# Kernel optimization log

Hardware: AMD Instinct MI355X
Metric: run time of the kernel (lower is better)

Reference implementation:

```python
import jax, jax.numpy as jnp
import numpy as np

HIDDEN = 1024
HEADS = 16
HEAD_DIM = HIDDEN // HEADS
MAX_SEQ = 2048
BATCH = 2
SEQ = 2048


def setup_inputs() -> dict:
    key = jax.random.key(0)
    ks = jax.random.split(key, 6)
    x = jax.random.normal(ks[0], (BATCH, SEQ, HIDDEN), dtype=jnp.float32)
    # torch Linear params expressed as [in, out] weight + bias
    W1 = jax.random.normal(ks[1], (HIDDEN, 4 * HIDDEN), dtype=jnp.float32) * (HIDDEN ** -0.5)
    b1 = jnp.zeros((4 * HIDDEN,), dtype=jnp.float32)
    W2 = jax.random.normal(ks[2], (HIDDEN, HIDDEN), dtype=jnp.float32) * (HIDDEN ** -0.5)
    b2 = jnp.zeros((HIDDEN,), dtype=jnp.float32)
    rel_table = jax.random.normal(ks[3], (2 * MAX_SEQ - 1, HEADS), dtype=jnp.float32) * 0.02
    # causal mask [B, S, S]; True = keep
    attn_mask = jnp.broadcast_to(jnp.tril(jnp.ones((SEQ, SEQ), dtype=bool)), (BATCH, SEQ, SEQ))
    return {"x": x, "W1": W1, "b1": b1, "W2": W2, "b2": b2,
            "rel_table": rel_table, "attn_mask": attn_mask}


def reference(x, W1, b1, W2, b2, rel_table, attn_mask):
    B, S, H = x.shape
    # fused projection + SiLU, then chunk into U, Q, K, V
    activated = jax.nn.silu(jnp.einsum('bsh,hf->bsf', x, W1) + b1)
    U, Qp, Kp, Vp = jnp.split(activated, 4, axis=-1)
    # [B, nH, S, hd]
    def heads(t):
        return t.reshape(B, S, HEADS, HEAD_DIM).transpose(0, 2, 1, 3)
    Q, K, V = heads(Qp), heads(Kp), heads(Vp)
    scale = HEAD_DIM ** -0.5
    scores = jnp.einsum('bnqd,bnkd->bnqk', Q, K) * scale
    # relative position bias gather: idx[i,j] = i - j + MAX_SEQ - 1
    pos = jnp.arange(S)
    rel_idx = pos[:, None] - pos[None, :] + (MAX_SEQ - 1)  # [S, S]
    rel_bias = rel_table[rel_idx].transpose(2, 0, 1)[None]  # [1, nH, S, S]
    scores = scores + rel_bias
    attn = jax.nn.silu(scores)
    attn = jnp.where(attn_mask[:, None, :, :], attn, 0.0)
    out = jnp.einsum('bnqk,bnkd->bnqd', attn, V)
    out = out.transpose(0, 2, 1, 3).reshape(B, S, H)
    gated = out * U
    return jnp.einsum('bsh,hf->bsf', gated, W2) + b2
```

## Files before the change

kernel.cpp:

```cpp
#include <hip/hip_runtime.h>
#include <hip/hip_bf16.h>
#include <math.h>

#define HIDDEN   1024
#define HEADS    16
#define HEAD_DIM 64
#define SEQ      2048
#define BATCH    2
#define FDIM     4096
#define MTOT     4096
#define MAXSEQ   2048

typedef __bf16 bf16x8 __attribute__((ext_vector_type(8)));
typedef float  f32x4  __attribute__((ext_vector_type(4)));
typedef unsigned short u16;

__device__ __forceinline__ float silu_fast(float v) {
    return v * __builtin_amdgcn_rcpf(1.f + __expf(-v));
}

__device__ __forceinline__ u16 f2bf(float f) {
    union { float f; unsigned u; } v; v.f = f;
    unsigned r = v.u + 0x7FFFu + ((v.u >> 16) & 1u);
    return (u16)(r >> 16);
}
__device__ __forceinline__ float bf2f(u16 b) {
    union { unsigned u; float f; } v; v.u = ((unsigned)b) << 16;
    return v.f;
}
__device__ __forceinline__ unsigned pk2(float a, float b) {
    union { __hip_bfloat162 h; unsigned u; } z;
    z.h = __float22bfloat162_rn(make_float2(a, b));
    return z.u;
}

__device__ __forceinline__ void gload16(const void* g, void* l) {
    __builtin_amdgcn_global_load_lds(
        (const __attribute__((address_space(1))) void*)g,
        (__attribute__((address_space(3))) void*)l, 16, 0, 0);
}

__global__ __launch_bounds__(256) void convert_x_kernel(
    const float* __restrict__ src, u16* __restrict__ dst)
{
    int idx = (blockIdx.x * 256 + threadIdx.x) * 8;
    float4 a = *(const float4*)&src[idx];
    float4 b = *(const float4*)&src[idx + 4];
    u16 h8[8] = {f2bf(a.x), f2bf(a.y), f2bf(a.z), f2bf(a.w),
                 f2bf(b.x), f2bf(b.y), f2bf(b.z), f2bf(b.w)};
    *(float4*)&dst[idx] = *(float4*)h8;
}

__global__ __launch_bounds__(256) void transpose_convert_kernel(
    const float* __restrict__ W, u16* __restrict__ Wt, int rows, int cols)
{
    __shared__ u16 T[64][72];
    const int tid = threadIdx.x;
    const int r0 = blockIdx.y * 64, c0 = blockIdx.x * 64;
#pragma unroll
    for (int l = 0; l < 4; ++l) {
        int idx = tid + l * 256;
        int row = idx >> 4;
        int c4  = (idx & 15) * 4;
        float4 v = *(const float4*)&W[(size_t)(r0 + row) * cols + c0 + c4];
        T[c4 + 0][row] = f2bf(v.x);
        T[c4 + 1][row] = f2bf(v.y);
        T[c4 + 2][row] = f2bf(v.z);
        T[c4 + 3][row] = f2bf(v.w);
    }
    __syncthreads();
#pragma unroll
    for (int l = 0; l < 2; ++l) {
        int idx = tid + l * 256;
        int row = idx >> 3;
        int cb  = (idx & 7) * 8;
        *(float4*)&Wt[(size_t)(c0 + row) * rows + r0 + cb] = *(float4*)&T[row][cb];
    }
}

#define GEMM_CORE(A_PTR, BT_PTR, KDIM, BM_, BN_, WMW, WNW)                     \
    enum { MTI = (BM_) / (WMW) / 16, NTI = (BN_) / (WNW) / 16,                 \
           ACH = (BM_) / 8, BCH = (BN_) / 8 };                                 \
    __shared__ __align__(16) u16 As[(BM_) * 64];                               \
    __shared__ __align__(16) u16 Bs[(BN_) * 64];                               \
    const int tid  = threadIdx.x;                                              \
    const int lane = tid & 63;                                                 \
    const int w    = tid >> 6;                                                 \
    const int wm   = w % (WMW), wn = w / (WMW);                                \
    const int l16  = lane & 15, quad = lane >> 4;                              \
    const int m0   = blockIdx.y * (BM_);                                       \
    const int n0   = blockIdx.x * (BN_);                                       \
    const int srow = lane >> 3;                                                \
    const int scol = (lane & 7) * 8;                                           \
    f32x4 acc[MTI][NTI];                                                       \
    _Pragma("unroll")                                                          \
    for (int mt = 0; mt < MTI; ++mt)                                           \
        _Pragma("unroll")                                                      \
        for (int nt = 0; nt < NTI; ++nt)                                       \
            acc[mt][nt] = (f32x4){0.f, 0.f, 0.f, 0.f};                         \
    for (int k0 = 0; k0 < (KDIM); k0 += 64) {                                  \
        __syncthreads();                                                       \
        _Pragma("unroll")                                                      \
        for (int ci = w; ci < ACH; ci += 4) {                                  \
            unsigned off = __builtin_amdgcn_readfirstlane(ci * 1024);          \
            gload16(&(A_PTR)[(size_t)(m0 + ci * 8 + srow) * (KDIM) + k0 + scol],\
                    (char*)As + off);                                          \
        }                                                                      \
        _Pragma("unroll")                                                      \
        for (int ci = w; ci < BCH; ci += 4) {                                  \
            unsigned off = __builtin_amdgcn_readfirstlane(ci * 1024);          \
            gload16(&(BT_PTR)[(size_t)(n0 + ci * 8 + srow) * (KDIM) + k0 + scol],\
                    (char*)Bs + off);                                          \
        }                                                                      \
        __syncthreads();                                                       \
        _Pragma("unroll")                                                      \
        for (int kc = 0; kc < 2; ++kc) {                                       \
            bf16x8 af[MTI], bfr[NTI];                                          \
            _Pragma("unroll")                                                  \
            for (int t = 0; t < MTI; ++t)                                      \
                af[t]  = *(const bf16x8*)&As[(wm * (BM_ / WMW) + t * 16 + l16) \
                                             * 64 + kc * 32 + quad * 8];       \
            _Pragma("unroll")                                                  \
            for (int t = 0; t < NTI; ++t)                                      \
                bfr[t] = *(const bf16x8*)&Bs[(wn * (BN_ / WNW) + t * 16 + l16) \
                                             * 64 + kc * 32 + quad * 8];       \
            _Pragma("unroll")                                                  \
            for (int mt = 0; mt < MTI; ++mt)                                   \
                _Pragma("unroll")                                              \
                for (int nt = 0; nt < NTI; ++nt)                               \
                    acc[mt][nt] = __builtin_amdgcn_mfma_f32_16x16x32_bf16(     \
                        bfr[nt], af[mt], acc[mt][nt], 0, 0, 0);                \
        }                                                                      \
    }

__global__ __launch_bounds__(256) void gemm1_mfma_kernel(
    const u16* __restrict__ A, const u16* __restrict__ Bt,
    const float* __restrict__ b1,
    u16* __restrict__ Ub, u16* __restrict__ Qh,
    u16* __restrict__ Kh, u16* __restrict__ Vh)
{
    GEMM_CORE(A, Bt, HIDDEN, 128, 128, 2, 2)

    const int chunk = n0 >> 10;
    u16* dstbase = (chunk == 0) ? Ub : (chunk == 1) ? Qh : (chunk == 2) ? Kh : Vh;
    const float postscale = (chunk == 1) ? 0.125f : 1.0f;

    float4 bias4[NTI]; int nloc[NTI];
#pragma unroll
    for (int nt = 0; nt < NTI; ++nt) {
        int nb = n0 + wn * 64 + nt * 16 + quad * 4;
        bias4[nt] = *(const float4*)&b1[nb];
        nloc[nt] = nb & 1023;
    }
#pragma unroll
    for (int mt = 0; mt < MTI; ++mt) {
        int m  = m0 + wm * 64 + mt * 16 + l16;
        int bb = m >> 11, s = m & 2047;
#pragma unroll
        for (int nt = 0; nt < NTI; ++nt) {
            float v0 = silu_fast(acc[mt][nt][0] + bias4[nt].x) * postscale;
            float v1 = silu_fast(acc[mt][nt][1] + bias4[nt].y) * postscale;
            float v2 = silu_fast(acc[mt][nt][2] + bias4[nt].z) * postscale;
            float v3 = silu_fast(acc[mt][nt][3] + bias4[nt].w) * postscale;
            uint2 pk = make_uint2(pk2(v0, v1), pk2(v2, v3));
            size_t o;
            if (chunk == 0) {
                o = (size_t)m * 1024 + nloc[nt];
            } else {
                int h = nloc[nt] >> 6, d = nloc[nt] & 63;
                o = (size_t)(((bb * HEADS + h) * SEQ) + s) * HEAD_DIM + d;
            }
            *(uint2*)&dstbase[o] = pk;
        }
    }
}

__global__ __launch_bounds__(256) void gemm2_mfma_kernel(
    const u16* __restrict__ A, const u16* __restrict__ Bt,
    const float* __restrict__ b2, float* __restrict__ Out)
{
    GEMM_CORE(A, Bt, HIDDEN, 64, 128, 1, 4)

    float4 bias4[NTI]; int nb[NTI];
#pragma unroll
    for (int nt = 0; nt < NTI; ++nt) {
        nb[nt] = n0 + wn * 32 + nt * 16 + quad * 4;
        bias4[nt] = *(const float4*)&b2[nb[nt]];
    }
#pragma unroll
    for (int mt = 0; mt < MTI; ++mt) {
        int m = m0 + mt * 16 + l16;
#pragma unroll
        for (int nt = 0; nt < NTI; ++nt) {
            float4 vv;
            vv.x = acc[mt][nt][0] + bias4[nt].x;
            vv.y = acc[mt][nt][1] + bias4[nt].y;
            vv.z = acc[mt][nt][2] + bias4[nt].z;
            vv.w = acc[mt][nt][3] + bias4[nt].w;
            *(float4*)&Out[(size_t)m * 1024 + nb[nt]] = vv;
        }
    }
}

#define PS 72

__global__ __launch_bounds__(256, 4) void attn_mfma_kernel(
    const u16* __restrict__ Qh, const u16* __restrict__ Kh,
    const u16* __restrict__ Vh, const float* __restrict__ rel,
    const u16* __restrict__ Ub, u16* __restrict__ G)
{
    __shared__ u16 Ks[64][PS];
    __shared__ u16 Vt[64][PS];
    __shared__ u16 Ps[64][PS];
    __shared__ float rel_sh[128];

    const int tid  = threadIdx.x;
    const int lane = tid & 63;
    const int w    = tid >> 6;
    const int quad = lane >> 4;
    const int l16  = lane & 15;

    const int bid   = blockIdx.x;
    const int x5    = bid & 31;
    const int h     = (bid >> 5) & 15;
    const int bb    = bid >> 9;
    const int phase = (bid >> 8) & 1;
    const int qt    = phase ? (31 - x5) : x5;
    const int q0    = qt * 64;

    const u16* Kg = Kh + (size_t)((bb * HEADS + h) * SEQ) * HEAD_DIM;
    const u16* Vg = Vh + (size_t)((bb * HEADS + h) * SEQ) * HEAD_DIM;
    const u16* Qg = Qh + (size_t)((bb * HEADS + h) * SEQ + q0) * HEAD_DIM;

    const int qrow = w * 16 + l16;
    bf16x8 qa0 = *(const bf16x8*)&Qg[qrow * HEAD_DIM + quad * 8];
    bf16x8 qa1 = *(const bf16x8*)&Qg[qrow * HEAD_DIM + 32 + quad * 8];

    const int k_r = tid >> 3,      k_c = (tid & 7) * 8;
    const int v_k = (tid & 31) * 2, v_d = (tid >> 5) * 8;

    float4 kreg0 = *(const float4*)&Kg[(size_t)k_r * HEAD_DIM + k_c];
    float4 kreg1 = *(const float4*)&Kg[(size_t)(k_r + 32) * HEAD_DIM + k_c];
    float4 vreg0 = *(const float4*)&Vg[(size_t)v_k * HEAD_DIM + v_d];
    float4 vreg1 = *(const float4*)&Vg[(size_t)(v_k + 1) * HEAD_DIM + v_d];
    float  relreg = 0.f;
    if (tid < 127) relreg = rel[(size_t)(q0 + 1984 + tid) * HEADS + h];

    f32x4 o[4];
#pragma unroll
    for (int dt = 0; dt < 4; ++dt) o[dt] = (f32x4){0.f, 0.f, 0.f, 0.f};

    for (int kt = 0; kt <= qt; ++kt) {
        *(float4*)&Ks[k_r][k_c]      = kreg0;
        *(float4*)&Ks[k_r + 32][k_c] = kreg1;
        {
            union { float4 f; u16 u[8]; } a0, a1;
            a0.f = vreg0; a1.f = vreg1;
#pragma unroll
            for (int i = 0; i < 8; ++i)
                *(unsigned*)&Vt[v_d + i][v_k] =
                    (unsigned)a0.u[i] | ((unsigned)a1.u[i] << 16);
        }
        if (tid < 127) rel_sh[tid] = relreg;
        __syncthreads();

        if (kt < qt) {
            const int kn = (kt + 1) * 64;
            kreg0 = *(const float4*)&Kg[(size_t)(kn + k_r) * HEAD_DIM + k_c];
            kreg1 = *(const float4*)&Kg[(size_t)(kn + k_r + 32) * HEAD_DIM + k_c];
            vreg0 = *(const float4*)&Vg[(size_t)(kn + v_k) * HEAD_DIM + v_d];
            vreg1 = *(const float4*)&Vg[(size_t)(kn + v_k + 1) * HEAD_DIM + v_d];
            if (tid < 127)
                relreg = rel[(size_t)(q0 - kn + 1984 + tid) * HEADS + h];
        }

        const int qrel = q0 - kt * 64 + qrow;

#pragma unroll
        for (int ct = 0; ct < 4; ++ct) {
            bf16x8 ka0 = *(const bf16x8*)&Ks[ct * 16 + l16][quad * 8];
            bf16x8 ka1 = *(const bf16x8*)&Ks[ct * 16 + l16][32 + quad * 8];
            f32x4 sc = {0.f, 0.f, 0.f, 0.f};
            sc = __builtin_amdgcn_mfma_f32_16x16x32_bf16(ka0, qa0, sc, 0, 0, 0);
            sc = __builtin_amdgcn_mfma_f32_16x16x32_bf16(ka1, qa1, sc, 0, 0, 0);
            float p[4];
#pragma unroll
            for (int r = 0; r < 4; ++r) {
                int kloc = ct * 16 + quad * 4 + r;
                float s  = sc[r] + rel_sh[qrow - kloc + 63];
                p[r] = (qrel - kloc >= 0) ? silu_fast(s) : 0.f;
            }
            uint2 pk = make_uint2(pk2(p[0], p[1]), pk2(p[2], p[3]));
            *(uint2*)&Ps[qrow][ct * 16 + quad * 4] = pk;
        }

        bf16x8 pa0 = *(const bf16x8*)&Ps[qrow][quad * 8];
        bf16x8 pa1 = *(const bf16x8*)&Ps[qrow][32 + quad * 8];
#pragma unroll
        for (int dt = 0; dt < 4; ++dt) {
            bf16x8 vb0 = *(const bf16x8*)&Vt[dt * 16 + l16][quad * 8];
            bf16x8 vb1 = *(const bf16x8*)&Vt[dt * 16 + l16][32 + quad * 8];
            o[dt] = __builtin_amdgcn_mfma_f32_16x16x32_bf16(pa0, vb0, o[dt], 0, 0, 0);
            o[dt] = __builtin_amdgcn_mfma_f32_16x16x32_bf16(pa1, vb1, o[dt], 0, 0, 0);
        }
        __syncthreads();
    }

#pragma unroll
    for (int dt = 0; dt < 4; ++dt)
#pragma unroll
        for (int r = 0; r < 4; ++r) {
            int q = q0 + w * 16 + quad * 4 + r;
            size_t base = (size_t)(bb * SEQ + q) * HIDDEN +
                          h * HEAD_DIM + dt * 16 + l16;
            float u = bf2f(Ub[base]);
            G[base] = f2bf(o[dt][r] * u);
        }
}

extern "C" void kernel_launch(void* const* d_in, const int* in_sizes, int n_in,
                              void* d_out, int out_size, void* d_ws, size_t ws_size,
                              hipStream_t stream)
{
    const float* X   = (const float*)d_in[0];
    const float* W1  = (const float*)d_in[1];
    const float* b1  = (const float*)d_in[2];
    const float* W2  = (const float*)d_in[3];
    const float* b2  = (const float*)d_in[4];
    const float* rel = (const float*)d_in[5];
    float* out = (float*)d_out;

    const size_t MH = (size_t)MTOT * HIDDEN;
    u16* Ub  = (u16*)d_ws;
    u16* Qh  = Ub  + MH;
    u16* Kh  = Qh  + MH;
    u16* Vh  = Kh  + MH;
    u16* G   = Vh  + MH;
    u16* Xb  = G   + MH;
    u16* W1t = Xb  + MH;
    u16* W2t = W1t + MH;

    convert_x_kernel<<<MTOT * HIDDEN / 2048, 256, 0, stream>>>(X, Xb);
    transpose_convert_kernel<<<dim3(FDIM / 64, HIDDEN / 64), 256, 0, stream>>>(
        W1, W1t, HIDDEN, FDIM);
    transpose_convert_kernel<<<dim3(HIDDEN / 64, HIDDEN / 64), 256, 0, stream>>>(
        W2, W2t, HIDDEN, HIDDEN);
    gemm1_mfma_kernel<<<dim3(FDIM / 128, MTOT / 128), 256, 0, stream>>>(
        Xb, W1t, b1, Ub, Qh, Kh, Vh);
    attn_mfma_kernel<<<dim3(1024), 256, 0, stream>>>(
        Qh, Kh, Vh, rel, Ub, G);
    gemm2_mfma_kernel<<<dim3(HIDDEN / 128, MTOT / 64), 256, 0, stream>>>(
        G, W2t, b2, out);
}
```

Before: 253.7 us.

## Restructure attention into single-wave blocks reading K/V directly from global

The attention kernel is rewritten so each 64-thread block handles 32 query rows and streams K and a pre-transposed V directly from global memory into MFMA operands. This removes the shared-memory staging and the block-wide barriers. GEMM1 now writes V transposed (d-major), and a new small kernel transposes the relative-position table so each block can load a contiguous bias band into LDS. The diagonal tile is handled separately so masking only happens there. The trade-off is more global and L2 traffic per block, scalar strided stores for V in the GEMM1 epilogue, and lower per-block reuse of K/V.

Result: slower. 279.0 us (+10.0%).

```diff
diff --git a/kernel.cpp b/kernel.cpp
--- a/kernel.cpp
+++ b/kernel.cpp
@@ -75,6 +75,21 @@
         int row = idx >> 3;
         int cb  = (idx & 7) * 8;
         *(float4*)&Wt[(size_t)(c0 + row) * rows + r0 + cb] = *(float4*)&T[row][cb];
+    }
+}
+
+__global__ __launch_bounds__(256) void rel_transpose_kernel(
+    const float* __restrict__ rel, float* __restrict__ rel_t)
+{
+    int dp = blockIdx.x * 256 + threadIdx.x;
+    if (dp < 2 * MAXSEQ - 1) {
+        float v[16];
+#pragma unroll
+        for (int i = 0; i < 4; ++i)
+            *(float4*)&v[i * 4] = *(const float4*)&rel[dp * 16 + i * 4];
+#pragma unroll
+        for (int h = 0; h < 16; ++h)
+            rel_t[h * 4096 + dp] = v[h];
     }
 }
 
@@ -137,12 +152,11 @@
     const u16* __restrict__ A, const u16* __restrict__ Bt,
     const float* __restrict__ b1,
     u16* __restrict__ Ub, u16* __restrict__ Qh,
-    u16* __restrict__ Kh, u16* __restrict__ Vh)
+    u16* __restrict__ Kh, u16* __restrict__ VtG)
 {
     GEMM_CORE(A, Bt, HIDDEN, 128, 128, 2, 2)
 
     const int chunk = n0 >> 10;
-    u16* dstbase = (chunk == 0) ? Ub : (chunk == 1) ? Qh : (chunk == 2) ? Kh : Vh;
     const float postscale = (chunk == 1) ? 0.125f : 1.0f;
 
     float4 bias4[NTI]; int nloc[NTI];
@@ -162,15 +176,27 @@
             float v1 = silu_fast(acc[mt][nt][1] + bias4[nt].y) * postscale;
             float v2 = silu_fast(acc[mt][nt][2] + bias4[nt].z) * postscale;
             float v3 = silu_fast(acc[mt][nt][3] + bias4[nt].w) * postscale;
-            uint2 pk = make_uint2(pk2(v0, v1), pk2(v2, v3));
-            size_t o;
-            if (chunk == 0) {
-                o = (size_t)m * 1024 + nloc[nt];
+            if (chunk == 3) {
+                int hh = nloc[nt] >> 6, d = nloc[nt] & 63;
+                size_t vb = ((size_t)((bb * 16 + hh) * 64 + d)) * 2048 + s;
+                VtG[vb]            = f2bf(v0);
+                VtG[vb + 2048]     = f2bf(v1);
+                VtG[vb + 2 * 2048] = f2bf(v2);
+                VtG[vb + 3 * 2048] = f2bf(v3);
             } else {
-                int h = nloc[nt] >> 6, d = nloc[nt] & 63;
-                o = (size_t)(((bb * HEADS + h) * SEQ) + s) * HEAD_DIM + d;
+                uint2 pk = make_uint2(pk2(v0, v1), pk2(v2, v3));
+                size_t o;
+                u16* dstbase;
+                if (chunk == 0) {
+                    dstbase = Ub;
+                    o = (size_t)m * 1024 + nloc[nt];
+                } else {
+                    dstbase = (chunk == 1) ? Qh : Kh;
+                    int hh = nloc[nt] >> 6, d = nloc[nt] & 63;
+                    o = (size_t)(((bb * HEADS + hh) * SEQ) + s) * HEAD_DIM + d;
+                }
+                *(uint2*)&dstbase[o] = pk;
             }
-            *(uint2*)&dstbase[o] = pk;
         }
     }
 }
@@ -202,119 +228,170 @@
     }
 }
 
-#define PS 72
-
-__global__ __launch_bounds__(256, 4) void attn_mfma_kernel(
+#define PSB 88
+
+__global__ __launch_bounds__(64, 2) void attn_mfma_kernel(
     const u16* __restrict__ Qh, const u16* __restrict__ Kh,
-    const u16* __restrict__ Vh, const float* __restrict__ rel,
+    const u16* __restrict__ VtG, const float* __restrict__ rel_t,
     const u16* __restrict__ Ub, u16* __restrict__ G)
 {
-    __shared__ u16 Ks[64][PS];
-    __shared__ u16 Vt[64][PS];
-    __shared__ u16 Ps[64][PS];
-    __shared__ float rel_sh[128];
-
-    const int tid  = threadIdx.x;
-    const int lane = tid & 63;
-    const int w    = tid >> 6;
-    const int quad = lane >> 4;
-    const int l16  = lane & 15;
-
-    const int bid   = blockIdx.x;
-    const int x5    = bid & 31;
-    const int h     = (bid >> 5) & 15;
-    const int bb    = bid >> 9;
-    const int phase = (bid >> 8) & 1;
-    const int qt    = phase ? (31 - x5) : x5;
-    const int q0    = qt * 64;
-
-    const u16* Kg = Kh + (size_t)((bb * HEADS + h) * SEQ) * HEAD_DIM;
-    const u16* Vg = Vh + (size_t)((bb * HEADS + h) * SEQ) * HEAD_DIM;
-    const u16* Qg = Qh + (size_t)((bb * HEADS + h) * SEQ + q0) * HEAD_DIM;
-
-    const int qrow = w * 16 + l16;
-    bf16x8 qa0 = *(const bf16x8*)&Qg[qrow * HEAD_DIM + quad * 8];
-    bf16x8 qa1 = *(const bf16x8*)&Qg[qrow * HEAD_DIM + 32 + quad * 8];
-
-    const int k_r = tid >> 3,      k_c = (tid & 7) * 8;
-    const int v_k = (tid & 31) * 2, v_d = (tid >> 5) * 8;
-
-    float4 kreg0 = *(const float4*)&Kg[(size_t)k_r * HEAD_DIM + k_c];
-    float4 kreg1 = *(const float4*)&Kg[(size_t)(k_r + 32) * HEAD_DIM + k_c];
-    float4 vreg0 = *(const float4*)&Vg[(size_t)v_k * HEAD_DIM + v_d];
-    float4 vreg1 = *(const float4*)&Vg[(size_t)(v_k + 1) * HEAD_DIM + v_d];
-    float  relreg = 0.f;
-    if (tid < 127) relreg = rel[(size_t)(q0 + 1984 + tid) * HEADS + h];
-
-    f32x4 o[4];
-#pragma unroll
-    for (int dt = 0; dt < 4; ++dt) o[dt] = (f32x4){0.f, 0.f, 0.f, 0.f};
-
-    for (int kt = 0; kt <= qt; ++kt) {
-        *(float4*)&Ks[k_r][k_c]      = kreg0;
-        *(float4*)&Ks[k_r + 32][k_c] = kreg1;
-        {
-            union { float4 f; u16 u[8]; } a0, a1;
-            a0.f = vreg0; a1.f = vreg1;
-#pragma unroll
-            for (int i = 0; i < 8; ++i)
-                *(unsigned*)&Vt[v_d + i][v_k] =
-                    (unsigned)a0.u[i] | ((unsigned)a1.u[i] << 16);
-        }
-        if (tid < 127) rel_sh[tid] = relreg;
-        __syncthreads();
-
-        if (kt < qt) {
-            const int kn = (kt + 1) * 64;
-            kreg0 = *(const float4*)&Kg[(size_t)(kn + k_r) * HEAD_DIM + k_c];
-            kreg1 = *(const float4*)&Kg[(size_t)(kn + k_r + 32) * HEAD_DIM + k_c];
-            vreg0 = *(const float4*)&Vg[(size_t)(kn + v_k) * HEAD_DIM + v_d];
-            vreg1 = *(const float4*)&Vg[(size_t)(kn + v_k + 1) * HEAD_DIM + v_d];
-            if (tid < 127)
-                relreg = rel[(size_t)(q0 - kn + 1984 + tid) * HEADS + h];
-        }
-
-        const int qrel = q0 - kt * 64 + qrow;
-
+    __shared__ __align__(16) u16   Ps[32][PSB];
+    __shared__ __align__(16) float relb[2080];
+
+    const int lane = threadIdx.x;
+    const int quad = lane >> 4, l16 = lane & 15;
+
+    const int bid = blockIdx.x;
+    const int c   = bid & 255;
+    const int kk_ = bid >> 8;
+    const int f   = kk_ & 1, j = kk_ >> 1;
+    const int h   = c & 15;
+    const int bb  = (c >> 4) & 1;
+    const int s2  = (c >> 5) & 7;
+    const int u   = (j << 3) | s2;
+    const int sig = f ? (63 - u) : u;
+    const int qt  = sig >> 1;
+    const int p   = sig & 1;
+    const int q0  = qt * 64;
+    const int qs  = sig * 32;
+
+    const u16* Kg = Kh  + (size_t)((bb * 16 + h) * 2048) * 64;
+    const u16* Vg = VtG + (size_t)((bb * 16 + h) * 64) * 2048;
+    const u16* Qg = Qh  + (size_t)((bb * 16 + h) * 2048 + qs) * 64;
+
+    const int wqA = p * 2, wqB = p * 2 + 1;
+
+    bf16x8 qaA0 = *(const bf16x8*)&Qg[l16 * 64 + quad * 8];
+    bf16x8 qaA1 = *(const bf16x8*)&Qg[l16 * 64 + 32 + quad * 8];
+    bf16x8 qaB0 = *(const bf16x8*)&Qg[(16 + l16) * 64 + quad * 8];
+    bf16x8 qaB1 = *(const bf16x8*)&Qg[(16 + l16) * 64 + 32 + quad * 8];
+
+    {
+        const float* relrow = rel_t + h * 4096 + (MAXSEQ - 1 - 15);
+        const int bandsz = qs + 47;
+        for (int base = lane * 4; base < bandsz; base += 256)
+            *(float4*)&relb[base] = *(const float4*)&relrow[base];
+    }
+
+    const int ibq = l16 - quad * 4 + 15;
+
+    f32x4 oA[4], oB[4];
+#pragma unroll
+    for (int dt = 0; dt < 4; ++dt) {
+        oA[dt] = (f32x4){0.f, 0.f, 0.f, 0.f};
+        oB[dt] = (f32x4){0.f, 0.f, 0.f, 0.f};
+    }
+
+    for (int kt = 0; kt < qt; ++kt) {
+        const u16* Kt = Kg + (size_t)(kt * 64) * 64;
+        const int ibA = (q0 - kt * 64) + wqA * 16 + ibq;
+        const int ibB = ibA + 16;
 #pragma unroll
         for (int ct = 0; ct < 4; ++ct) {
-            bf16x8 ka0 = *(const bf16x8*)&Ks[ct * 16 + l16][quad * 8];
-            bf16x8 ka1 = *(const bf16x8*)&Ks[ct * 16 + l16][32 + quad * 8];
-            f32x4 sc = {0.f, 0.f, 0.f, 0.f};
-            sc = __builtin_amdgcn_mfma_f32_16x16x32_bf16(ka0, qa0, sc, 0, 0, 0);
-            sc = __builtin_amdgcn_mfma_f32_16x16x32_bf16(ka1, qa1, sc, 0, 0, 0);
-            float p[4];
+            bf16x8 ka0 = *(const bf16x8*)&Kt[(ct * 16 + l16) * 64 + quad * 8];
+            bf16x8 ka1 = *(const bf16x8*)&Kt[(ct * 16 + l16) * 64 + 32 + quad * 8];
+            f32x4 sA = {0.f, 0.f, 0.f, 0.f}, sB = {0.f, 0.f, 0.f, 0.f};
+            sA = __builtin_amdgcn_mfma_f32_16x16x32_bf16(ka0, qaA0, sA, 0, 0, 0);
+            sA = __builtin_amdgcn_mfma_f32_16x16x32_bf16(ka1, qaA1, sA, 0, 0, 0);
+            sB = __builtin_amdgcn_mfma_f32_16x16x32_bf16(ka0, qaB0, sB, 0, 0, 0);
+            sB = __builtin_amdgcn_mfma_f32_16x16x32_bf16(ka1, qaB1, sB, 0, 0, 0);
+            float pA[4], pB[4];
 #pragma unroll
             for (int r = 0; r < 4; ++r) {
-                int kloc = ct * 16 + quad * 4 + r;
-                float s  = sc[r] + rel_sh[qrow - kloc + 63];
-                p[r] = (qrel - kloc >= 0) ? silu_fast(s) : 0.f;
+                pA[r] = silu_fast(sA[r] + relb[ibA - ct * 16 - r]);
+                pB[r] = silu_fast(sB[r] + relb[ibB - ct * 16 - r]);
             }
-            uint2 pk = make_uint2(pk2(p[0], p[1]), pk2(p[2], p[3]));
-            *(uint2*)&Ps[qrow][ct * 16 + quad * 4] = pk;
-        }
-
-        bf16x8 pa0 = *(const bf16x8*)&Ps[qrow][quad * 8];
-        bf16x8 pa1 = *(const bf16x8*)&Ps[qrow][32 + quad * 8];
+            *(uint2*)&Ps[l16][ct * 16 + quad * 4] =
+                make_uint2(pk2(pA[0], pA[1]), pk2(pA[2], pA[3]));
+            *(uint2*)&Ps[16 + l16][ct * 16 + quad * 4] =
+                make_uint2(pk2(pB[0], pB[1]), pk2(pB[2], pB[3]));
+        }
+        bf16x8 paA0 = *(const bf16x8*)&Ps[l16][quad * 8];
+        bf16x8 paA1 = *(const bf16x8*)&Ps[l16][32 + quad * 8];
+        bf16x8 paB0 = *(const bf16x8*)&Ps[16 + l16][quad * 8];
+        bf16x8 paB1 = *(const bf16x8*)&Ps[16 + l16][32 + quad * 8];
+        const u16* Vk = Vg + kt * 64;
 #pragma unroll
         for (int dt = 0; dt < 4; ++dt) {
-            bf16x8 vb0 = *(const bf16x8*)&Vt[dt * 16 + l16][quad * 8];
-            bf16x8 vb1 = *(const bf16x8*)&Vt[dt * 16 + l16][32 + quad * 8];
-            o[dt] = __builtin_amdgcn_mfma_f32_16x16x32_bf16(pa0, vb0, o[dt], 0, 0, 0);
-            o[dt] = __builtin_amdgcn_mfma_f32_16x16x32_bf16(pa1, vb1, o[dt], 0, 0, 0);
-        }
-        __syncthreads();
+            bf16x8 vb0 = *(const bf16x8*)&Vk[(dt * 16 + l16) * 2048 + quad * 8];
+            bf16x8 vb1 = *(const bf16x8*)&Vk[(dt * 16 + l16) * 2048 + 32 + quad * 8];
+            oA[dt] = __builtin_amdgcn_mfma_f32_16x16x32_bf16(paA0, vb0, oA[dt], 0, 0, 0);
+            oA[dt] = __builtin_amdgcn_mfma_f32_16x16x32_bf16(paA1, vb1, oA[dt], 0, 0, 0);
+            oB[dt] = __builtin_amdgcn_mfma_f32_16x16x32_bf16(paB0, vb0, oB[dt], 0, 0, 0);
+            oB[dt] = __builtin_amdgcn_mfma_f32_16x16x32_bf16(paB1, vb1, oB[dt], 0, 0, 0);
+        }
+    }
+
+    {
+        const u16* Kt = Kg + (size_t)(qt * 64) * 64;
+        const int ibA = wqA * 16 + ibq;
+        const int ibB = ibA + 16;
+#pragma unroll
+        for (int ct = 0; ct < 4; ++ct) {
+            if (ct <= wqB) {
+                bf16x8 ka0 = *(const bf16x8*)&Kt[(ct * 16 + l16) * 64 + quad * 8];
+                bf16x8 ka1 = *(const bf16x8*)&Kt[(ct * 16 + l16) * 64 + 32 + quad * 8];
+                f32x4 sB = {0.f, 0.f, 0.f, 0.f};
+                sB = __builtin_amdgcn_mfma_f32_16x16x32_bf16(ka0, qaB0, sB, 0, 0, 0);
+                sB = __builtin_amdgcn_mfma_f32_16x16x32_bf16(ka1, qaB1, sB, 0, 0, 0);
+                float pB[4];
+#pragma unroll
+                for (int r = 0; r < 4; ++r) {
+                    int ix = ibB - ct * 16 - r;
+                    float sv = sB[r] + relb[ix];
+                    pB[r] = (ix >= 15) ? silu_fast(sv) : 0.f;
+                }
+                *(uint2*)&Ps[16 + l16][ct * 16 + quad * 4] =
+                    make_uint2(pk2(pB[0], pB[1]), pk2(pB[2], pB[3]));
+                if (ct <= wqA) {
+                    f32x4 sA = {0.f, 0.f, 0.f, 0.f};
+                    sA = __builtin_amdgcn_mfma_f32_16x16x32_bf16(ka0, qaA0, sA, 0, 0, 0);
+                    sA = __builtin_amdgcn_mfma_f32_16x16x32_bf16(ka1, qaA1, sA, 0, 0, 0);
+                    float pA[4];
+#pragma unroll
+                    for (int r = 0; r < 4; ++r) {
+                        int ix = ibA - ct * 16 - r;
+                        float sv = sA[r] + relb[ix];
+                        pA[r] = (ix >= 15) ? silu_fast(sv) : 0.f;
+                    }
+                    *(uint2*)&Ps[l16][ct * 16 + quad * 4] =
+                        make_uint2(pk2(pA[0], pA[1]), pk2(pA[2], pA[3]));
+                } else {
+                    *(uint2*)&Ps[l16][ct * 16 + quad * 4] = make_uint2(0u, 0u);
+                }
+            }
+        }
+        const u16* Vk = Vg + qt * 64;
+        bf16x8 paA0 = *(const bf16x8*)&Ps[l16][quad * 8];
+        bf16x8 paB0 = *(const bf16x8*)&Ps[16 + l16][quad * 8];
+#pragma unroll
+        for (int dt = 0; dt < 4; ++dt) {
+            bf16x8 vb0 = *(const bf16x8*)&Vk[(dt * 16 + l16) * 2048 + quad * 8];
+            oA[dt] = __builtin_amdgcn_mfma_f32_16x16x32_bf16(paA0, vb0, oA[dt], 0, 0, 0);
+            oB[dt] = __builtin_amdgcn_mfma_f32_16x16x32_bf16(paB0, vb0, oB[dt], 0, 0, 0);
+        }
+        if (p) {
+            bf16x8 paA1 = *(const bf16x8*)&Ps[l16][32 + quad * 8];
+            bf16x8 paB1 = *(const bf16x8*)&Ps[16 + l16][32 + quad * 8];
+#pragma unroll
+            for (int dt = 0; dt < 4; ++dt) {
+                bf16x8 vb1 = *(const bf16x8*)&Vk[(dt * 16 + l16) * 2048 + 32 + quad * 8];
+                oA[dt] = __builtin_amdgcn_mfma_f32_16x16x32_bf16(paA1, vb1, oA[dt], 0, 0, 0);
+                oB[dt] = __builtin_amdgcn_mfma_f32_16x16x32_bf16(paB1, vb1, oB[dt], 0, 0, 0);
+            }
+        }
     }
 
 #pragma unroll
     for (int dt = 0; dt < 4; ++dt)
 #pragma unroll
         for (int r = 0; r < 4; ++r) {
-            int q = q0 + w * 16 + quad * 4 + r;
-            size_t base = (size_t)(bb * SEQ + q) * HIDDEN +
-                          h * HEAD_DIM + dt * 16 + l16;
-            float u = bf2f(Ub[base]);
-            G[base] = f2bf(o[dt][r] * u);
+            int qA = qs + quad * 4 + r;
+            int qB = qA + 16;
+            size_t baseA = (size_t)(bb * 2048 + qA) * 1024 + h * 64 + dt * 16 + l16;
+            size_t baseB = (size_t)(bb * 2048 + qB) * 1024 + h * 64 + dt * 16 + l16;
+            G[baseA] = f2bf(oA[dt][r] * bf2f(Ub[baseA]));
+            G[baseB] = f2bf(oB[dt][r] * bf2f(Ub[baseB]));
         }
 }
 
@@ -331,24 +408,26 @@
     float* out = (float*)d_out;
 
     const size_t MH = (size_t)MTOT * HIDDEN;
-    u16* Ub  = (u16*)d_ws;
-    u16* Qh  = Ub  + MH;
-    u16* Kh  = Qh  + MH;
-    u16* Vh  = Kh  + MH;
-    u16* G   = Vh  + MH;
-    u16* Xb  = G   + MH;
-    u16* W1t = Xb  + MH;
-    u16* W2t = W1t + MH;
+    u16*   Ub    = (u16*)d_ws;
+    u16*   Qh    = Ub  + MH;
+    u16*   Kh    = Qh  + MH;
+    u16*   VtG   = Kh  + MH;
+    u16*   Gbuf  = VtG + MH;
+    u16*   Xb    = Gbuf + MH;
+    u16*   W1t   = Xb  + MH;
+    u16*   W2t   = W1t + MH;
+    float* rel_t = (float*)(W2t + (size_t)HIDDEN * HIDDEN);
 
     convert_x_kernel<<<MTOT * HIDDEN / 2048, 256, 0, stream>>>(X, Xb);
     transpose_convert_kernel<<<dim3(FDIM / 64, HIDDEN / 64), 256, 0, stream>>>(
         W1, W1t, HIDDEN, FDIM);
     transpose_convert_kernel<<<dim3(HIDDEN / 64, HIDDEN / 64), 256, 0, stream>>>(
         W2, W2t, HIDDEN, HIDDEN);
+    rel_transpose_kernel<<<16, 256, 0, stream>>>(rel, rel_t);
     gemm1_mfma_kernel<<<dim3(FDIM / 128, MTOT / 128), 256, 0, stream>>>(
-        Xb, W1t, b1, Ub, Qh, Kh, Vh);
-    attn_mfma_kernel<<<dim3(1024), 256, 0, stream>>>(
-        Qh, Kh, Vh, rel, Ub, G);
+        Xb, W1t, b1, Ub, Qh, Kh, VtG);
+    attn_mfma_kernel<<<2048, 64, 0, stream>>>(
+        Qh, Kh, VtG, rel_t, Ub, Gbuf);
     gemm2_mfma_kernel<<<dim3(HIDDEN / 128, MTOT / 64), 256, 0, stream>>>(
-        G, W2t, b2, out);
-}
+        Gbuf, W2t, b2, out);
+}
```

## Fuse X conversion into GEMM1 and emit V pre-transposed for attention

Applied to the files above, without the earlier changes.

Removes the separate fp32-to-bf16 conversion kernel for X. GEMM1 now reads fp32 X directly and converts it while staging the tile into shared memory. GEMM1 also writes V in a transposed [b,h,d,s] layout, so the attention kernel loads V fragments straight from global memory and no longer transposes them through LDS. The cost is a heavier A-tile load in GEMM1 (twice the bytes, synchronous instead of global_load_lds), scattered 2-byte stores for V, and uncached per-iteration global V loads in attention with no prefetch.

Result: slower. 324.2 us (+27.8%).

```diff
diff --git a/kernel.cpp b/kernel.cpp
--- a/kernel.cpp
+++ b/kernel.cpp
@@ -38,17 +38,6 @@
     __builtin_amdgcn_global_load_lds(
         (const __attribute__((address_space(1))) void*)g,
         (__attribute__((address_space(3))) void*)l, 16, 0, 0);
-}
-
-__global__ __launch_bounds__(256) void convert_x_kernel(
-    const float* __restrict__ src, u16* __restrict__ dst)
-{
-    int idx = (blockIdx.x * 256 + threadIdx.x) * 8;
-    float4 a = *(const float4*)&src[idx];
-    float4 b = *(const float4*)&src[idx + 4];
-    u16 h8[8] = {f2bf(a.x), f2bf(a.y), f2bf(a.z), f2bf(a.w),
-                 f2bf(b.x), f2bf(b.y), f2bf(b.z), f2bf(b.w)};
-    *(float4*)&dst[idx] = *(float4*)h8;
 }
 
 __global__ __launch_bounds__(256) void transpose_convert_kernel(
@@ -134,43 +123,109 @@
     }
 
 __global__ __launch_bounds__(256) void gemm1_mfma_kernel(
-    const u16* __restrict__ A, const u16* __restrict__ Bt,
+    const float* __restrict__ X, const u16* __restrict__ Bt,
     const float* __restrict__ b1,
     u16* __restrict__ Ub, u16* __restrict__ Qh,
-    u16* __restrict__ Kh, u16* __restrict__ Vh)
-{
-    GEMM_CORE(A, Bt, HIDDEN, 128, 128, 2, 2)
+    u16* __restrict__ Kh, u16* __restrict__ VtG)
+{
+    enum { MTI = 4, NTI = 4 };
+    __shared__ __align__(16) u16 As[128 * 64];
+    __shared__ __align__(16) u16 Bs[128 * 64];
+    const int tid  = threadIdx.x;
+    const int lane = tid & 63;
+    const int w    = tid >> 6;
+    const int wm   = w & 1, wn = w >> 1;
+    const int l16  = lane & 15, quad = lane >> 4;
+    const int m0   = blockIdx.y * 128;
+    const int n0   = blockIdx.x * 128;
+    const int srow = lane >> 3;
+    const int scol = (lane & 7) * 8;
+
+    f32x4 acc[4][4];
+#pragma unroll
+    for (int mt = 0; mt < 4; ++mt)
+#pragma unroll
+        for (int nt = 0; nt < 4; ++nt)
+            acc[mt][nt] = (f32x4){0.f, 0.f, 0.f, 0.f};
+
+    for (int k0 = 0; k0 < HIDDEN; k0 += 64) {
+        __syncthreads();
+#pragma unroll
+        for (int ci = w; ci < 16; ci += 4) {
+            const float* src = &X[(size_t)(m0 + ci * 8 + srow) * HIDDEN + k0 + scol];
+            float4 x0 = *(const float4*)src;
+            float4 x1 = *(const float4*)(src + 4);
+            uint4 pk = make_uint4(pk2(x0.x, x0.y), pk2(x0.z, x0.w),
+                                  pk2(x1.x, x1.y), pk2(x1.z, x1.w));
+            *(uint4*)&As[(ci * 8 + srow) * 64 + scol] = pk;
+        }
+#pragma unroll
+        for (int ci = w; ci < 16; ci += 4) {
+            unsigned off = __builtin_amdgcn_readfirstlane(ci * 1024);
+            gload16(&Bt[(size_t)(n0 + ci * 8 + srow) * HIDDEN + k0 + scol],
+                    (char*)Bs + off);
+        }
+        __syncthreads();
+#pragma unroll
+        for (int kc = 0; kc < 2; ++kc) {
+            bf16x8 af[4], bfr[4];
+#pragma unroll
+            for (int t = 0; t < 4; ++t) {
+                af[t]  = *(const bf16x8*)&As[(wm * 64 + t * 16 + l16) * 64 +
+                                             kc * 32 + quad * 8];
+                bfr[t] = *(const bf16x8*)&Bs[(wn * 64 + t * 16 + l16) * 64 +
+                                             kc * 32 + quad * 8];
+            }
+#pragma unroll
+            for (int mt = 0; mt < 4; ++mt)
+#pragma unroll
+                for (int nt = 0; nt < 4; ++nt)
+                    acc[mt][nt] = __builtin_amdgcn_mfma_f32_16x16x32_bf16(
+                        bfr[nt], af[mt], acc[mt][nt], 0, 0, 0);
+        }
+    }
 
     const int chunk = n0 >> 10;
-    u16* dstbase = (chunk == 0) ? Ub : (chunk == 1) ? Qh : (chunk == 2) ? Kh : Vh;
     const float postscale = (chunk == 1) ? 0.125f : 1.0f;
 
-    float4 bias4[NTI]; int nloc[NTI];
-#pragma unroll
-    for (int nt = 0; nt < NTI; ++nt) {
+    float4 bias4[4]; int nloc[4];
+#pragma unroll
+    for (int nt = 0; nt < 4; ++nt) {
         int nb = n0 + wn * 64 + nt * 16 + quad * 4;
         bias4[nt] = *(const float4*)&b1[nb];
         nloc[nt] = nb & 1023;
     }
 #pragma unroll
-    for (int mt = 0; mt < MTI; ++mt) {
+    for (int mt = 0; mt < 4; ++mt) {
         int m  = m0 + wm * 64 + mt * 16 + l16;
         int bb = m >> 11, s = m & 2047;
 #pragma unroll
-        for (int nt = 0; nt < NTI; ++nt) {
+        for (int nt = 0; nt < 4; ++nt) {
             float v0 = silu_fast(acc[mt][nt][0] + bias4[nt].x) * postscale;
             float v1 = silu_fast(acc[mt][nt][1] + bias4[nt].y) * postscale;
             float v2 = silu_fast(acc[mt][nt][2] + bias4[nt].z) * postscale;
             float v3 = silu_fast(acc[mt][nt][3] + bias4[nt].w) * postscale;
-            uint2 pk = make_uint2(pk2(v0, v1), pk2(v2, v3));
-            size_t o;
-            if (chunk == 0) {
-                o = (size_t)m * 1024 + nloc[nt];
+            if (chunk == 3) {
+                int hh = nloc[nt] >> 6, d = nloc[nt] & 63;
+                size_t vb = ((size_t)((bb * 16 + hh) * 64 + d)) * 2048 + s;
+                VtG[vb]            = f2bf(v0);
+                VtG[vb + 2048]     = f2bf(v1);
+                VtG[vb + 2 * 2048] = f2bf(v2);
+                VtG[vb + 3 * 2048] = f2bf(v3);
             } else {
-                int h = nloc[nt] >> 6, d = nloc[nt] & 63;
-                o = (size_t)(((bb * HEADS + h) * SEQ) + s) * HEAD_DIM + d;
+                uint2 pk = make_uint2(pk2(v0, v1), pk2(v2, v3));
+                size_t o;
+                u16* dstbase;
+                if (chunk == 0) {
+                    dstbase = Ub;
+                    o = (size_t)m * 1024 + nloc[nt];
+                } else {
+                    dstbase = (chunk == 1) ? Qh : Kh;
+                    int hh = nloc[nt] >> 6, d = nloc[nt] & 63;
+                    o = (size_t)(((bb * HEADS + hh) * SEQ) + s) * HEAD_DIM + d;
+                }
+                *(uint2*)&dstbase[o] = pk;
             }
-            *(uint2*)&dstbase[o] = pk;
         }
     }
 }
@@ -206,11 +261,10 @@
 
 __global__ __launch_bounds__(256, 4) void attn_mfma_kernel(
     const u16* __restrict__ Qh, const u16* __restrict__ Kh,
-    const u16* __restrict__ Vh, const float* __restrict__ rel,
+    const u16* __restrict__ VtG, const float* __restrict__ rel,
     const u16* __restrict__ Ub, u16* __restrict__ G)
 {
     __shared__ u16 Ks[64][PS];
-    __shared__ u16 Vt[64][PS];
     __shared__ u16 Ps[64][PS];
     __shared__ float rel_sh[128];
 
@@ -228,21 +282,18 @@
     const int qt    = phase ? (31 - x5) : x5;
     const int q0    = qt * 64;
 
-    const u16* Kg = Kh + (size_t)((bb * HEADS + h) * SEQ) * HEAD_DIM;
-    const u16* Vg = Vh + (size_t)((bb * HEADS + h) * SEQ) * HEAD_DIM;
-    const u16* Qg = Qh + (size_t)((bb * HEADS + h) * SEQ + q0) * HEAD_DIM;
+    const u16* Kg = Kh  + (size_t)((bb * HEADS + h) * SEQ) * HEAD_DIM;
+    const u16* Vg = VtG + (size_t)((bb * HEADS + h) * HEAD_DIM) * SEQ;
+    const u16* Qg = Qh  + (size_t)((bb * HEADS + h) * SEQ + q0) * HEAD_DIM;
 
     const int qrow = w * 16 + l16;
     bf16x8 qa0 = *(const bf16x8*)&Qg[qrow * HEAD_DIM + quad * 8];
     bf16x8 qa1 = *(const bf16x8*)&Qg[qrow * HEAD_DIM + 32 + quad * 8];
 
-    const int k_r = tid >> 3,      k_c = (tid & 7) * 8;
-    const int v_k = (tid & 31) * 2, v_d = (tid >> 5) * 8;
+    const int k_r = tid >> 3, k_c = (tid & 7) * 8;
 
     float4 kreg0 = *(const float4*)&Kg[(size_t)k_r * HEAD_DIM + k_c];
     float4 kreg1 = *(const float4*)&Kg[(size_t)(k_r + 32) * HEAD_DIM + k_c];
-    float4 vreg0 = *(const float4*)&Vg[(size_t)v_k * HEAD_DIM + v_d];
-    float4 vreg1 = *(const float4*)&Vg[(size_t)(v_k + 1) * HEAD_DIM + v_d];
     float  relreg = 0.f;
     if (tid < 127) relreg = rel[(size_t)(q0 + 1984 + tid) * HEADS + h];
 
@@ -251,30 +302,28 @@
     for (int dt = 0; dt < 4; ++dt) o[dt] = (f32x4){0.f, 0.f, 0.f, 0.f};
 
     for (int kt = 0; kt <= qt; ++kt) {
+        const int k0 = kt * 64;
         *(float4*)&Ks[k_r][k_c]      = kreg0;
         *(float4*)&Ks[k_r + 32][k_c] = kreg1;
-        {
-            union { float4 f; u16 u[8]; } a0, a1;
-            a0.f = vreg0; a1.f = vreg1;
-#pragma unroll
-            for (int i = 0; i < 8; ++i)
-                *(unsigned*)&Vt[v_d + i][v_k] =
-                    (unsigned)a0.u[i] | ((unsigned)a1.u[i] << 16);
-        }
         if (tid < 127) rel_sh[tid] = relreg;
         __syncthreads();
 
         if (kt < qt) {
-            const int kn = (kt + 1) * 64;
+            const int kn = k0 + 64;
             kreg0 = *(const float4*)&Kg[(size_t)(kn + k_r) * HEAD_DIM + k_c];
             kreg1 = *(const float4*)&Kg[(size_t)(kn + k_r + 32) * HEAD_DIM + k_c];
-            vreg0 = *(const float4*)&Vg[(size_t)(kn + v_k) * HEAD_DIM + v_d];
-            vreg1 = *(const float4*)&Vg[(size_t)(kn + v_k + 1) * HEAD_DIM + v_d];
             if (tid < 127)
                 relreg = rel[(size_t)(q0 - kn + 1984 + tid) * HEADS + h];
         }
 
-        const int qrel = q0 - kt * 64 + qrow;
+        bf16x8 vb[4][2];
+#pragma unroll
+        for (int dt = 0; dt < 4; ++dt) {
+            vb[dt][0] = *(const bf16x8*)&Vg[(dt * 16 + l16) * SEQ + k0 + quad * 8];
+            vb[dt][1] = *(const bf16x8*)&Vg[(dt * 16 + l16) * SEQ + k0 + 32 + quad * 8];
+        }
+
+        const int qrel = q0 - k0 + qrow;
 
 #pragma unroll
         for (int ct = 0; ct < 4; ++ct) {
@@ -298,10 +347,8 @@
         bf16x8 pa1 = *(const bf16x8*)&Ps[qrow][32 + quad * 8];
 #pragma unroll
         for (int dt = 0; dt < 4; ++dt) {
-            bf16x8 vb0 = *(const bf16x8*)&Vt[dt * 16 + l16][quad * 8];
-            bf16x8 vb1 = *(const bf16x8*)&Vt[dt * 16 + l16][32 + quad * 8];
-            o[dt] = __builtin_amdgcn_mfma_f32_16x16x32_bf16(pa0, vb0, o[dt], 0, 0, 0);
-            o[dt] = __builtin_amdgcn_mfma_f32_16x16x32_bf16(pa1, vb1, o[dt], 0, 0, 0);
+            o[dt] = __builtin_amdgcn_mfma_f32_16x16x32_bf16(pa0, vb[dt][0], o[dt], 0, 0, 0);
+            o[dt] = __builtin_amdgcn_mfma_f32_16x16x32_bf16(pa1, vb[dt][1], o[dt], 0, 0, 0);
         }
         __syncthreads();
     }
@@ -331,24 +378,22 @@
     float* out = (float*)d_out;
 
     const size_t MH = (size_t)MTOT * HIDDEN;
-    u16* Ub  = (u16*)d_ws;
-    u16* Qh  = Ub  + MH;
-    u16* Kh  = Qh  + MH;
-    u16* Vh  = Kh  + MH;
-    u16* G   = Vh  + MH;
-    u16* Xb  = G   + MH;
-    u16* W1t = Xb  + MH;
-    u16* W2t = W1t + MH;
-
-    convert_x_kernel<<<MTOT * HIDDEN / 2048, 256, 0, stream>>>(X, Xb);
+    u16* Ub   = (u16*)d_ws;
+    u16* Qh   = Ub  + MH;
+    u16* Kh   = Qh  + MH;
+    u16* VtG  = Kh  + MH;
+    u16* Gbuf = VtG + MH;
+    u16* W1t  = Gbuf + MH;
+    u16* W2t  = W1t + MH;
+
     transpose_convert_kernel<<<dim3(FDIM / 64, HIDDEN / 64), 256, 0, stream>>>(
         W1, W1t, HIDDEN, FDIM);
     transpose_convert_kernel<<<dim3(HIDDEN / 64, HIDDEN / 64), 256, 0, stream>>>(
         W2, W2t, HIDDEN, HIDDEN);
     gemm1_mfma_kernel<<<dim3(FDIM / 128, MTOT / 128), 256, 0, stream>>>(
-        Xb, W1t, b1, Ub, Qh, Kh, Vh);
+        X, W1t, b1, Ub, Qh, Kh, VtG);
     attn_mfma_kernel<<<dim3(1024), 256, 0, stream>>>(
-        Qh, Kh, Vh, rel, Ub, G);
+        Qh, Kh, VtG, rel, Ub, Gbuf);
     gemm2_mfma_kernel<<<dim3(HIDDEN / 128, MTOT / 64), 256, 0, stream>>>(
-        G, W2t, b2, out);
-}
+        Gbuf, W2t, b2, out);
+}
```

## Process two 64-key tiles per barrier pair and skip masking off-diagonal

Applied to the files above, without the earlier changes.

The attention loop now stages two 64-row K/V tiles (128 keys) per iteration in shared memory, halving the number of __syncthreads barriers and prefetch phases. The causal mask and comparison are applied only on the diagonal tile, and off-diagonal tiles compute SiLU without a per-element check. The cost is more registers for double-tile prefetch and larger shared memory, with launch bounds lowered from 4 to 3 blocks per CU, which may reduce occupancy.

New measurement: 250.1 us. No clear change (-1.4%).

```diff
diff --git a/kernel.cpp b/kernel.cpp
--- a/kernel.cpp
+++ b/kernel.cpp
@@ -202,17 +202,15 @@
     }
 }
 
-#define PS 72
-
-__global__ __launch_bounds__(256, 4) void attn_mfma_kernel(
+__global__ __launch_bounds__(256, 3) void attn_mfma_kernel(
     const u16* __restrict__ Qh, const u16* __restrict__ Kh,
     const u16* __restrict__ Vh, const float* __restrict__ rel,
     const u16* __restrict__ Ub, u16* __restrict__ G)
 {
-    __shared__ u16 Ks[64][PS];
-    __shared__ u16 Vt[64][PS];
-    __shared__ u16 Ps[64][PS];
-    __shared__ float rel_sh[128];
+    __shared__ u16 Ks[128][72];
+    __shared__ u16 Vt[64][136];
+    __shared__ u16 Ps[64][72];
+    __shared__ float rel_sh[192];
 
     const int tid  = threadIdx.x;
     const int lane = tid & 63;
@@ -236,75 +234,127 @@
     bf16x8 qa0 = *(const bf16x8*)&Qg[qrow * HEAD_DIM + quad * 8];
     bf16x8 qa1 = *(const bf16x8*)&Qg[qrow * HEAD_DIM + 32 + quad * 8];
 
-    const int k_r = tid >> 3,      k_c = (tid & 7) * 8;
+    const int k_r = tid >> 3,       k_c = (tid & 7) * 8;
     const int v_k = (tid & 31) * 2, v_d = (tid >> 5) * 8;
 
-    float4 kreg0 = *(const float4*)&Kg[(size_t)k_r * HEAD_DIM + k_c];
-    float4 kreg1 = *(const float4*)&Kg[(size_t)(k_r + 32) * HEAD_DIM + k_c];
-    float4 vreg0 = *(const float4*)&Vg[(size_t)v_k * HEAD_DIM + v_d];
-    float4 vreg1 = *(const float4*)&Vg[(size_t)(v_k + 1) * HEAD_DIM + v_d];
-    float  relreg = 0.f;
-    if (tid < 127) relreg = rel[(size_t)(q0 + 1984 + tid) * HEADS + h];
+    float4 kA0 = *(const float4*)&Kg[(size_t)k_r * 64 + k_c];
+    float4 kA1 = *(const float4*)&Kg[(size_t)(k_r + 32) * 64 + k_c];
+    float4 vA0 = *(const float4*)&Vg[(size_t)v_k * 64 + v_d];
+    float4 vA1 = *(const float4*)&Vg[(size_t)(v_k + 1) * 64 + v_d];
+    float4 kB0, kB1, vB0, vB1;
+    if (qt >= 1) {
+        kB0 = *(const float4*)&Kg[(size_t)(64 + k_r) * 64 + k_c];
+        kB1 = *(const float4*)&Kg[(size_t)(64 + k_r + 32) * 64 + k_c];
+        vB0 = *(const float4*)&Vg[(size_t)(64 + v_k) * 64 + v_d];
+        vB1 = *(const float4*)&Vg[(size_t)(64 + v_k + 1) * 64 + v_d];
+    }
+    float relreg = 0.f;
+    if (tid < 191) relreg = rel[(size_t)(q0 + 1920 + tid) * HEADS + h];
 
     f32x4 o[4];
 #pragma unroll
     for (int dt = 0; dt < 4; ++dt) o[dt] = (f32x4){0.f, 0.f, 0.f, 0.f};
 
-    for (int kt = 0; kt <= qt; ++kt) {
-        *(float4*)&Ks[k_r][k_c]      = kreg0;
-        *(float4*)&Ks[k_r + 32][k_c] = kreg1;
+#define ATTN_CHUNK(KOFS, RELOFS, DIAG, QREL)                                   \
+    {                                                                          \
+        _Pragma("unroll")                                                      \
+        for (int ct = 0; ct < 4; ++ct) {                                       \
+            bf16x8 ka0 = *(const bf16x8*)&Ks[(KOFS) + ct * 16 + l16][quad * 8];\
+            bf16x8 ka1 = *(const bf16x8*)&Ks[(KOFS) + ct * 16 + l16][32 + quad * 8];\
+            f32x4 sc = {0.f, 0.f, 0.f, 0.f};                                   \
+            sc = __builtin_amdgcn_mfma_f32_16x16x32_bf16(ka0, qa0, sc, 0, 0, 0);\
+            sc = __builtin_amdgcn_mfma_f32_16x16x32_bf16(ka1, qa1, sc, 0, 0, 0);\
+            const int ib = qrow - ct * 16 - quad * 4 + (RELOFS);               \
+            float p[4];                                                        \
+            _Pragma("unroll")                                                  \
+            for (int r = 0; r < 4; ++r) {                                      \
+                float s = sc[r] + rel_sh[ib - r];                              \
+                if (DIAG) {                                                    \
+                    int kloc = ct * 16 + quad * 4 + r;                         \
+                    p[r] = ((QREL) - kloc >= 0) ? silu_fast(s) : 0.f;          \
+                } else {                                                       \
+                    p[r] = silu_fast(s);                                       \
+                }                                                              \
+            }                                                                  \
+            *(uint2*)&Ps[qrow][ct * 16 + quad * 4] =                           \
+                make_uint2(pk2(p[0], p[1]), pk2(p[2], p[3]));                  \
+        }                                                                      \
+        bf16x8 pa0 = *(const bf16x8*)&Ps[qrow][quad * 8];                      \
+        bf16x8 pa1 = *(const bf16x8*)&Ps[qrow][32 + quad * 8];                 \
+        const int vo = (KOFS);                                                 \
+        _Pragma("unroll")                                                      \
+        for (int dt = 0; dt < 4; ++dt) {                                       \
+            bf16x8 vb0 = *(const bf16x8*)&Vt[dt * 16 + l16][vo + quad * 8];    \
+            bf16x8 vb1 = *(const bf16x8*)&Vt[dt * 16 + l16][vo + 32 + quad * 8];\
+            o[dt] = __builtin_amdgcn_mfma_f32_16x16x32_bf16(pa0, vb0, o[dt], 0, 0, 0);\
+            o[dt] = __builtin_amdgcn_mfma_f32_16x16x32_bf16(pa1, vb1, o[dt], 0, 0, 0);\
+        }                                                                      \
+    }
+
+    for (int ip = 0; 2 * ip <= qt; ++ip) {
+        const int kp = ip * 128;
+        const bool hasB = (2 * ip + 1 <= qt);
+
+        *(float4*)&Ks[k_r][k_c]      = kA0;
+        *(float4*)&Ks[k_r + 32][k_c] = kA1;
         {
             union { float4 f; u16 u[8]; } a0, a1;
-            a0.f = vreg0; a1.f = vreg1;
+            a0.f = vA0; a1.f = vA1;
 #pragma unroll
             for (int i = 0; i < 8; ++i)
                 *(unsigned*)&Vt[v_d + i][v_k] =
                     (unsigned)a0.u[i] | ((unsigned)a1.u[i] << 16);
         }
-        if (tid < 127) rel_sh[tid] = relreg;
+        if (hasB) {
+            *(float4*)&Ks[64 + k_r][k_c]      = kB0;
+            *(float4*)&Ks[64 + k_r + 32][k_c] = kB1;
+            union { float4 f; u16 u[8]; } a0, a1;
+            a0.f = vB0; a1.f = vB1;
+#pragma unroll
+            for (int i = 0; i < 8; ++i)
+                *(unsigned*)&Vt[v_d + i][64 + v_k] =
+                    (unsigned)a0.u[i] | ((unsigned)a1.u[i] << 16);
+        }
+        if (tid < 191) rel_sh[tid] = relreg;
         __syncthreads();
 
-        if (kt < qt) {
-            const int kn = (kt + 1) * 64;
-            kreg0 = *(const float4*)&Kg[(size_t)(kn + k_r) * HEAD_DIM + k_c];
-            kreg1 = *(const float4*)&Kg[(size_t)(kn + k_r + 32) * HEAD_DIM + k_c];
-            vreg0 = *(const float4*)&Vg[(size_t)(kn + v_k) * HEAD_DIM + v_d];
-            vreg1 = *(const float4*)&Vg[(size_t)(kn + v_k + 1) * HEAD_DIM + v_d];
-            if (tid < 127)
-                relreg = rel[(size_t)(q0 - kn + 1984 + tid) * HEADS + h];
-        }
-
-        const int qrel = q0 - kt * 64 + qrow;
-
-#pragma unroll
-        for (int ct = 0; ct < 4; ++ct) {
-            bf16x8 ka0 = *(const bf16x8*)&Ks[ct * 16 + l16][quad * 8];
-            bf16x8 ka1 = *(const bf16x8*)&Ks[ct * 16 + l16][32 + quad * 8];
-            f32x4 sc = {0.f, 0.f, 0.f, 0.f};
-            sc = __builtin_amdgcn_mfma_f32_16x16x32_bf16(ka0, qa0, sc, 0, 0, 0);
-            sc = __builtin_amdgcn_mfma_f32_16x16x32_bf16(ka1, qa1, sc, 0, 0, 0);
-            float p[4];
-#pragma unroll
-            for (int r = 0; r < 4; ++r) {
-                int kloc = ct * 16 + quad * 4 + r;
-                float s  = sc[r] + rel_sh[qrow - kloc + 63];
-                p[r] = (qrel - kloc >= 0) ? silu_fast(s) : 0.f;
+        {
+            const int nk0 = 2 * ip + 2;
+            if (nk0 <= qt) {
+                const int b0 = nk0 * 64;
+                kA0 = *(const float4*)&Kg[(size_t)(b0 + k_r) * 64 + k_c];
+                kA1 = *(const float4*)&Kg[(size_t)(b0 + k_r + 32) * 64 + k_c];
+                vA0 = *(const float4*)&Vg[(size_t)(b0 + v_k) * 64 + v_d];
+                vA1 = *(const float4*)&Vg[(size_t)(b0 + v_k + 1) * 64 + v_d];
+                if (tid < 191)
+                    relreg = rel[(size_t)(q0 - kp - 128 + 1920 + tid) * HEADS + h];
+                if (nk0 + 1 <= qt) {
+                    const int b1 = b0 + 64;
+                    kB0 = *(const float4*)&Kg[(size_t)(b1 + k_r) * 64 + k_c];
+                    kB1 = *(const float4*)&Kg[(size_t)(b1 + k_r + 32) * 64 + k_c];
+                    vB0 = *(const float4*)&Vg[(size_t)(b1 + v_k) * 64 + v_d];
+                    vB1 = *(const float4*)&Vg[(size_t)(b1 + v_k + 1) * 64 + v_d];
+                }
             }
-            uint2 pk = make_uint2(pk2(p[0], p[1]), pk2(p[2], p[3]));
-            *(uint2*)&Ps[qrow][ct * 16 + quad * 4] = pk;
-        }
-
-        bf16x8 pa0 = *(const bf16x8*)&Ps[qrow][quad * 8];
-        bf16x8 pa1 = *(const bf16x8*)&Ps[qrow][32 + quad * 8];
-#pragma unroll
-        for (int dt = 0; dt < 4; ++dt) {
-            bf16x8 vb0 = *(const bf16x8*)&Vt[dt * 16 + l16][quad * 8];
-            bf16x8 vb1 = *(const bf16x8*)&Vt[dt * 16 + l16][32 + quad * 8];
-            o[dt] = __builtin_amdgcn_mfma_f32_16x16x32_bf16(pa0, vb0, o[dt], 0, 0, 0);
-            o[dt] = __builtin_amdgcn_mfma_f32_16x16x32_bf16(pa1, vb1, o[dt], 0, 0, 0);
+        }
+
+        if (2 * ip == qt) {
+            const int qrel0 = q0 - kp + qrow;
+            ATTN_CHUNK(0, 127, true, qrel0)
+        } else {
+            ATTN_CHUNK(0, 127, false, 0)
+        }
+        if (hasB) {
+            if (2 * ip + 1 == qt) {
+                const int qrel1 = q0 - kp - 64 + qrow;
+                ATTN_CHUNK(64, 63, true, qrel1)
+            } else {
+                ATTN_CHUNK(64, 63, false, 0)
+            }
         }
         __syncthreads();
     }
+#undef ATTN_CHUNK
 
 #pragma unroll
     for (int dt = 0; dt < 4; ++dt)
@@ -331,14 +381,14 @@
     float* out = (float*)d_out;
 
     const size_t MH = (size_t)MTOT * HIDDEN;
-    u16* Ub  = (u16*)d_ws;
-    u16* Qh  = Ub  + MH;
-    u16* Kh  = Qh  + MH;
-    u16* Vh  = Kh  + MH;
-    u16* G   = Vh  + MH;
-    u16* Xb  = G   + MH;
-    u16* W1t = Xb  + MH;
-    u16* W2t = W1t + MH;
+    u16* Ub   = (u16*)d_ws;
+    u16* Qh   = Ub  + MH;
+    u16* Kh   = Qh  + MH;
+    u16* Vh   = Kh  + MH;
+    u16* Gbuf = Vh  + MH;
+    u16* Xb   = Gbuf + MH;
+    u16* W1t  = Xb  + MH;
+    u16* W2t  = W1t + MH;
 
     convert_x_kernel<<<MTOT * HIDDEN / 2048, 256, 0, stream>>>(X, Xb);
     transpose_convert_kernel<<<dim3(FDIM / 64, HIDDEN / 64), 256, 0, stream>>>(
@@ -348,7 +398,7 @@
     gemm1_mfma_kernel<<<dim3(FDIM / 128, MTOT / 128), 256, 0, stream>>>(
         Xb, W1t, b1, Ub, Qh, Kh, Vh);
     attn_mfma_kernel<<<dim3(1024), 256, 0, stream>>>(
-        Qh, Kh, Vh, rel, Ub, G);
+        Qh, Kh, Vh, rel, Ub, Gbuf);
     gemm2_mfma_kernel<<<dim3(HIDDEN / 128, MTOT / 64), 256, 0, stream>>>(
-        G, W2t, b2, out);
-}
+        Gbuf, W2t, b2, out);
+}
```
